# Performance work log

Hardware: AMD Instinct MI355X
Metric: run time of the kernel (lower is better)

The kernel has to match this reference:

```python
import jax, jax.numpy as jnp
import numpy as np

B, S, H, U = 32, 4096, 512, 512


def setup_inputs() -> dict:
    key = jax.random.key(0)
    ks = jax.random.split(key, 6)
    scale = 1.0 / np.sqrt(H)
    return {
        "query": jax.random.normal(ks[0], (B, H), dtype=jnp.float32),
        "values": jax.random.normal(ks[1], (B, S, H), dtype=jnp.float32),
        "W1": jax.random.normal(ks[2], (H, U), dtype=jnp.float32) * scale,
        "b1": jnp.zeros((U,), dtype=jnp.float32),
        "W2": jax.random.normal(ks[3], (H, U), dtype=jnp.float32) * scale,
        "b2": jnp.zeros((U,), dtype=jnp.float32),
        "va": jax.random.normal(ks[4], (U, 1), dtype=jnp.float32) * (1.0 / np.sqrt(U)),
        "bva": jnp.zeros((1,), dtype=jnp.float32),
    }


def reference(query, values, W1, b1, W2, b2, va, bva):
    # query: [B, H] -> [B, 1, U]; values: [B, S, H] -> [B, S, U]
    q_proj = jnp.einsum('bh,hu->bu', query, W1) + b1           # [B, U]
    v_proj = jnp.einsum('bsh,hu->bsu', values, W2) + b2        # [B, S, U]
    scores = jnp.einsum('bsu,uo->bso', jnp.tanh(q_proj[:, None, :] + v_proj), va) + bva  # [B, S, 1]
    attention_weights = jax.nn.softmax(scores, axis=1)         # [B, S, 1]
    context_vector = jnp.sum(attention_weights * values, axis=1)  # [B, H]
    return attention_weights, context_vector
```

## Files before the change

### kernel.cpp

```cpp
#include <hip/hip_runtime.h>
#include <hip/hip_bf16.h>
#include <stdint.h>

#define B_SZ 32
#define S_SZ 4096
#define H_SZ 512
#define U_SZ 512

typedef __attribute__((ext_vector_type(8))) _Float16 half8;
typedef __attribute__((ext_vector_type(4))) float floatx4;

__device__ __forceinline__ void async_copy16(const void* g, void* l) {
    __builtin_amdgcn_global_load_lds(
        (const __attribute__((address_space(1))) void*)g,
        (__attribute__((address_space(3))) void*)l, 16, 0, 0);
}

__global__ __launch_bounds__(256) void prep_kernel(
    const float* __restrict__ W2, const float* __restrict__ b1,
    const float* __restrict__ b2, const float* __restrict__ bva,
    const float* __restrict__ query, const float* __restrict__ W1,
    _Float16* __restrict__ W2s, float* __restrict__ qpb2,
    float* __restrict__ scores, float* __restrict__ ctx)
{
    const int t = threadIdx.x;
    const int bid = blockIdx.x;
    if (bid < 1024) {
        const int i = bid * 256 + t;
        const int k = i >> 9, n = i & 511;
        W2s[(k >> 5) * 16384 + ((k >> 3) & 3) * 4096 + n * 8 + (k & 7)] =
            (_Float16)W2[i];
    } else if (bid < 1536) {
        scores[(bid - 1024) * 256 + t] = *bva;
    } else if (bid < 1600) {
        ctx[(bid - 1536) * 256 + t] = 0.0f;
    } else {
        const int bq = bid - 1600;
        const int b = bq >> 1, uc = bq & 1;
        const int u = uc * 256 + t;
        const float* q  = query + b * H_SZ;
        const float* Wp = W1 + u;
        float a0 = 0.f, a1 = 0.f, a2 = 0.f, a3 = 0.f;
        for (int k = 0; k < 512; k += 4) {
            a0 = fmaf(q[k],     Wp[(size_t)k * U_SZ],       a0);
            a1 = fmaf(q[k + 1], Wp[(size_t)(k + 1) * U_SZ], a1);
            a2 = fmaf(q[k + 2], Wp[(size_t)(k + 2) * U_SZ], a2);
            a3 = fmaf(q[k + 3], Wp[(size_t)(k + 3) * U_SZ], a3);
        }
        qpb2[b * U_SZ + u] = (a0 + a1) + (a2 + a3) + b1[u] + b2[u];
    }
}

__global__ __launch_bounds__(256, 3) void scores_kernel(
    const float* __restrict__ values, const _Float16* __restrict__ W2s,
    const float* __restrict__ qpb2, const float* __restrict__ va,
    float* __restrict__ scores)
{
    __shared__ __align__(16) float    Albs[2][4096];
    __shared__ __align__(16) _Float16 Blbs[2][4096];
    __shared__ float red[256];

    const int t  = threadIdx.x;
    const int w  = t >> 6, l = t & 63;
    const int c  = l & 15, g4 = l >> 4;
    const int mh = w >> 1, nh = w & 1;
    const int n0 = (blockIdx.x & 3) * 128;
    const int m0 = (blockIdx.x >> 2) * 128;
    const int b  = m0 >> 12;

    floatx4 acc[4][4];
#pragma unroll
    for (int mt = 0; mt < 4; ++mt)
#pragma unroll
        for (int nt = 0; nt < 4; ++nt) acc[mt][nt] = (floatx4)(0.0f);

    const float*    Vb0 = values + (size_t)m0 * H_SZ;
    const _Float16* Wb0 = W2s + n0 * 8;

    auto stage = [&](int kb, int buf) {
        const float* Vb = Vb0 + kb * 32;
#pragma unroll
        for (int i = 0; i < 4; ++i) {
            const int j = t + i * 256;
            const int g = j >> 7, ml = j & 127;
            async_copy16(Vb + (size_t)ml * H_SZ + g * 4, &Albs[buf][j * 4]);
        }
        const _Float16* Wb = Wb0 + kb * 16384;
#pragma unroll
        for (int i = 0; i < 2; ++i) {
            const int j = t + i * 256;
            const int kq = j >> 7, nl = j & 127;
            async_copy16(Wb + kq * 4096 + nl * 8, &Blbs[buf][j * 8]);
        }
    };

    stage(0, 0);
    __syncthreads();

    for (int kb = 0; kb < 16; ++kb) {
        const int cur = kb & 1;
        if (kb < 15) stage(kb + 1, cur ^ 1);
        half8 af[4];
#pragma unroll
        for (int mt = 0; mt < 4; ++mt) {
            const int ml = mh * 64 + mt * 16 + c;
            float4 lo = *(const float4*)&Albs[cur][((2 * g4)     * 128 + ml) * 4];
            float4 hi = *(const float4*)&Albs[cur][((2 * g4 + 1) * 128 + ml) * 4];
            half8 a;
            a[0] = (_Float16)lo.x; a[1] = (_Float16)lo.y;
            a[2] = (_Float16)lo.z; a[3] = (_Float16)lo.w;
            a[4] = (_Float16)hi.x; a[5] = (_Float16)hi.y;
            a[6] = (_Float16)hi.z; a[7] = (_Float16)hi.w;
            af[mt] = a;
        }
        half8 bf[4];
#pragma unroll
        for (int nt = 0; nt < 4; ++nt) {
            const int nl = nh * 64 + nt * 16 + c;
            bf[nt] = *(const half8*)&Blbs[cur][(g4 * 128 + nl) * 8];
        }
#pragma unroll
        for (int mt = 0; mt < 4; ++mt)
#pragma unroll
            for (int nt = 0; nt < 4; ++nt)
                acc[mt][nt] = __builtin_amdgcn_mfma_f32_16x16x32_f16(
                    af[mt], bf[nt], acc[mt][nt], 0, 0, 0);
        __syncthreads();
    }

    float qv2[4], vv[4], vv2[4];
#pragma unroll
    for (int nt = 0; nt < 4; ++nt) {
        const int n = n0 + nh * 64 + nt * 16 + c;
        const float q = qpb2[b * U_SZ + n];
        const float v = va[n];
        qv2[nt] = 2.0f * q;
        vv[nt] = v;
        vv2[nt] = 2.0f * v;
    }
#pragma unroll
    for (int mt = 0; mt < 4; ++mt) {
#pragma unroll
        for (int r = 0; r < 4; ++r) {
            float p = 0.0f;
#pragma unroll
            for (int nt = 0; nt < 4; ++nt) {
                const float ex = __expf(fmaf(acc[mt][nt][r], 2.0f, qv2[nt]));
                const float rc = __builtin_amdgcn_rcpf(ex + 1.0f);
                p = fmaf(-vv2[nt], rc, p + vv[nt]);
            }
            p += __shfl_xor(p, 1);
            p += __shfl_xor(p, 2);
            p += __shfl_xor(p, 4);
            p += __shfl_xor(p, 8);
            if (c == 0)
                red[(mh * 64 + mt * 16 + g4 * 4 + r) * 2 + nh] = p;
        }
    }
    __syncthreads();
    if (t < 128)
        atomicAdd(&scores[m0 + t], red[t * 2] + red[t * 2 + 1]);
}

__global__ __launch_bounds__(1024) void sredux_kernel(
    const float* __restrict__ scores, float* __restrict__ ML)
{
    __shared__ float red[16];
    __shared__ float s_max;
    const int b = blockIdx.x;
    const int t = threadIdx.x;
    float4 v = *(const float4*)(scores + b * S_SZ + t * 4);
    float m = fmaxf(fmaxf(v.x, v.y), fmaxf(v.z, v.w));
#pragma unroll
    for (int o = 32; o > 0; o >>= 1) m = fmaxf(m, __shfl_xor(m, o));
    if ((t & 63) == 0) red[t >> 6] = m;
    __syncthreads();
    if (t == 0) {
        float mm = red[0];
        for (int i = 1; i < 16; ++i) mm = fmaxf(mm, red[i]);
        s_max = mm;
    }
    __syncthreads();
    const float mm = s_max;
    float s = __expf(v.x - mm) + __expf(v.y - mm) +
              __expf(v.z - mm) + __expf(v.w - mm);
#pragma unroll
    for (int o = 32; o > 0; o >>= 1) s += __shfl_xor(s, o);
    if ((t & 63) == 0) red[t >> 6] = s;
    __syncthreads();
    if (t == 0) {
        float ss = 0.0f;
        for (int i = 0; i < 16; ++i) ss += red[i];
        ML[b * 2] = mm;
        ML[b * 2 + 1] = ss;
    }
}

__global__ __launch_bounds__(256) void context_kernel(
    const float* __restrict__ values, const float* __restrict__ scores,
    const float* __restrict__ ML, float* __restrict__ out)
{
    __shared__ float wl[128];
    __shared__ __align__(16) float part[4][512];
    const int sc = blockIdx.x, b = blockIdx.y;
    const int t = threadIdx.x;
    const int s0 = sc * 128;
    const float M = ML[b * 2];
    const float rL = 1.0f / ML[b * 2 + 1];
    if (t < 32) {
        float4 sv = *(const float4*)(scores + b * S_SZ + s0 + t * 4);
        float4 wv;
        wv.x = __expf(sv.x - M) * rL; wv.y = __expf(sv.y - M) * rL;
        wv.z = __expf(sv.z - M) * rL; wv.w = __expf(sv.w - M) * rL;
        *(float4*)&wl[t * 4] = wv;
        *(float4*)(out + b * S_SZ + s0 + t * 4) = wv;
    }
    __syncthreads();

    const int g = t >> 6, l = t & 63;
    const float* vp = values + ((size_t)b * S_SZ + s0 + g * 32) * H_SZ + l * 4;
    float4 a00 = {0,0,0,0}, a01 = {0,0,0,0}, a10 = {0,0,0,0}, a11 = {0,0,0,0};
    for (int i = 0; i < 32; i += 2) {
        const float w0 = wl[g * 32 + i];
        const float w1 = wl[g * 32 + i + 1];
        const float* r0 = vp + (size_t)i * H_SZ;
        const float* r1 = r0 + H_SZ;
        float4 v00 = *(const float4*)(r0);
        float4 v01 = *(const float4*)(r0 + 256);
        float4 v10 = *(const float4*)(r1);
        float4 v11 = *(const float4*)(r1 + 256);
        a00.x = fmaf(w0, v00.x, a00.x); a00.y = fmaf(w0, v00.y, a00.y);
        a00.z = fmaf(w0, v00.z, a00.z); a00.w = fmaf(w0, v00.w, a00.w);
        a01.x = fmaf(w0, v01.x, a01.x); a01.y = fmaf(w0, v01.y, a01.y);
        a01.z = fmaf(w0, v01.z, a01.z); a01.w = fmaf(w0, v01.w, a01.w);
        a10.x = fmaf(w1, v10.x, a10.x); a10.y = fmaf(w1, v10.y, a10.y);
        a10.z = fmaf(w1, v10.z, a10.z); a10.w = fmaf(w1, v10.w, a10.w);
        a11.x = fmaf(w1, v11.x, a11.x); a11.y = fmaf(w1, v11.y, a11.y);
        a11.z = fmaf(w1, v11.z, a11.z); a11.w = fmaf(w1, v11.w, a11.w);
    }
    a00.x += a10.x; a00.y += a10.y; a00.z += a10.z; a00.w += a10.w;
    a01.x += a11.x; a01.y += a11.y; a01.z += a11.z; a01.w += a11.w;
    *(float4*)&part[g][l * 4] = a00;
    *(float4*)&part[g][256 + l * 4] = a01;
    __syncthreads();

    float* ctx = out + B_SZ * S_SZ;
#pragma unroll
    for (int rep = 0; rep < 2; ++rep) {
        const int h = rep * 256 + t;
        const float s = (part[0][h] + part[1][h]) + (part[2][h] + part[3][h]);
        atomicAdd(&ctx[b * H_SZ + h], s);
    }
}

extern "C" void kernel_launch(void* const* d_in, const int* in_sizes, int n_in,
                              void* d_out, int out_size, void* d_ws, size_t ws_size,
                              hipStream_t stream) {
    const float* query  = (const float*)d_in[0];
    const float* values = (const float*)d_in[1];
    const float* W1     = (const float*)d_in[2];
    const float* b1     = (const float*)d_in[3];
    const float* W2     = (const float*)d_in[4];
    const float* b2     = (const float*)d_in[5];
    const float* va     = (const float*)d_in[6];
    const float* bva    = (const float*)d_in[7];
    float* out = (float*)d_out;

    char* ws = (char*)d_ws;
    float*    qpb2   = (float*)ws;
    _Float16* W2s    = (_Float16*)(ws + 65536);
    float*    scores = (float*)(ws + 65536 + 524288);
    float*    ML     = (float*)(ws + 65536 + 2 * 524288);

    float* ctx = out + B_SZ * S_SZ;

    prep_kernel<<<1664, 256, 0, stream>>>(W2, b1, b2, bva, query, W1,
                                          W2s, qpb2, scores, ctx);
    scores_kernel<<<4096, 256, 0, stream>>>(values, W2s, qpb2, va, scores);
    sredux_kernel<<<32, 1024, 0, stream>>>(scores, ML);
    context_kernel<<<dim3(32, 32), 256, 0, stream>>>(values, scores, ML, out);
}
```

Before: 595.9 us.

## Pre-convert values to fp16 once and reuse it in the scores and context kernels

Adds a conversion pass in the prep kernel that writes an fp16 copy of values into the workspace. The scores GEMM is templated so it can stream fp16 A tiles straight into MFMA with half the LDS and no per-tile conversion, and its occupancy hint rises from 3 to 4. A new context kernel reads the fp16 copy. This cuts repeated fp32 traffic and conversion work, at the cost of an extra full pass over values and lower precision in the context sum. The fp16 path is used only when the workspace is large enough; otherwise the old fp32 path runs.

```diff
diff --git a/kernel.cpp b/kernel.cpp
--- a/kernel.cpp
+++ b/kernel.cpp
@@ -17,25 +17,39 @@
 }
 
 __global__ __launch_bounds__(256) void prep_kernel(
-    const float* __restrict__ W2, const float* __restrict__ b1,
-    const float* __restrict__ b2, const float* __restrict__ bva,
-    const float* __restrict__ query, const float* __restrict__ W1,
-    _Float16* __restrict__ W2s, float* __restrict__ qpb2,
-    float* __restrict__ scores, float* __restrict__ ctx)
+    const float* __restrict__ values, const float* __restrict__ W2,
+    const float* __restrict__ b1, const float* __restrict__ b2,
+    const float* __restrict__ bva, const float* __restrict__ query,
+    const float* __restrict__ W1, _Float16* __restrict__ W2s,
+    float* __restrict__ qpb2, float* __restrict__ scores,
+    float* __restrict__ ctx, _Float16* __restrict__ vf16, int nconv)
 {
     const int t = threadIdx.x;
     const int bid = blockIdx.x;
-    if (bid < 1024) {
-        const int i = bid * 256 + t;
+    if (bid < nconv) {
+        const size_t i = ((size_t)bid * 256 + t) * 8;
+        float4 v0 = *(const float4*)(values + i);
+        float4 v1 = *(const float4*)(values + i + 4);
+        half8 h;
+        h[0] = (_Float16)v0.x; h[1] = (_Float16)v0.y;
+        h[2] = (_Float16)v0.z; h[3] = (_Float16)v0.w;
+        h[4] = (_Float16)v1.x; h[5] = (_Float16)v1.y;
+        h[6] = (_Float16)v1.z; h[7] = (_Float16)v1.w;
+        *(half8*)(vf16 + i) = h;
+        return;
+    }
+    const int rb = bid - nconv;
+    if (rb < 1024) {
+        const int i = rb * 256 + t;
         const int k = i >> 9, n = i & 511;
         W2s[(k >> 5) * 16384 + ((k >> 3) & 3) * 4096 + n * 8 + (k & 7)] =
             (_Float16)W2[i];
-    } else if (bid < 1536) {
-        scores[(bid - 1024) * 256 + t] = *bva;
-    } else if (bid < 1600) {
-        ctx[(bid - 1536) * 256 + t] = 0.0f;
+    } else if (rb < 1536) {
+        scores[(rb - 1024) * 256 + t] = *bva;
+    } else if (rb < 1600) {
+        ctx[(rb - 1536) * 256 + t] = 0.0f;
     } else {
-        const int bq = bid - 1600;
+        const int bq = rb - 1600;
         const int b = bq >> 1, uc = bq & 1;
         const int u = uc * 256 + t;
         const float* q  = query + b * H_SZ;
@@ -51,12 +65,13 @@
     }
 }
 
-__global__ __launch_bounds__(256, 3) void scores_kernel(
-    const float* __restrict__ values, const _Float16* __restrict__ W2s,
+template <typename AT>
+__global__ __launch_bounds__(256, 4) void scores_kernel(
+    const AT* __restrict__ A, const _Float16* __restrict__ W2s,
     const float* __restrict__ qpb2, const float* __restrict__ va,
     float* __restrict__ scores)
 {
-    __shared__ __align__(16) float    Albs[2][4096];
+    __shared__ __align__(16) AT       Albs[2][4096];
     __shared__ __align__(16) _Float16 Blbs[2][4096];
     __shared__ float red[256];
 
@@ -74,16 +89,25 @@
 #pragma unroll
         for (int nt = 0; nt < 4; ++nt) acc[mt][nt] = (floatx4)(0.0f);
 
-    const float*    Vb0 = values + (size_t)m0 * H_SZ;
+    const AT*       Ab0 = A + (size_t)m0 * H_SZ;
     const _Float16* Wb0 = W2s + n0 * 8;
 
     auto stage = [&](int kb, int buf) {
-        const float* Vb = Vb0 + kb * 32;
-#pragma unroll
-        for (int i = 0; i < 4; ++i) {
-            const int j = t + i * 256;
-            const int g = j >> 7, ml = j & 127;
-            async_copy16(Vb + (size_t)ml * H_SZ + g * 4, &Albs[buf][j * 4]);
+        const AT* Vb = Ab0 + kb * 32;
+        if constexpr (sizeof(AT) == 4) {
+#pragma unroll
+            for (int i = 0; i < 4; ++i) {
+                const int j = t + i * 256;
+                const int g = j >> 7, ml = j & 127;
+                async_copy16(Vb + (size_t)ml * H_SZ + g * 4, &Albs[buf][j * 4]);
+            }
+        } else {
+#pragma unroll
+            for (int i = 0; i < 2; ++i) {
+                const int j = t + i * 256;
+                const int g = j >> 7, ml = j & 127;
+                async_copy16(Vb + (size_t)ml * H_SZ + g * 8, &Albs[buf][j * 8]);
+            }
         }
         const _Float16* Wb = Wb0 + kb * 16384;
 #pragma unroll
@@ -104,14 +128,18 @@
 #pragma unroll
         for (int mt = 0; mt < 4; ++mt) {
             const int ml = mh * 64 + mt * 16 + c;
-            float4 lo = *(const float4*)&Albs[cur][((2 * g4)     * 128 + ml) * 4];
-            float4 hi = *(const float4*)&Albs[cur][((2 * g4 + 1) * 128 + ml) * 4];
-            half8 a;
-            a[0] = (_Float16)lo.x; a[1] = (_Float16)lo.y;
-            a[2] = (_Float16)lo.z; a[3] = (_Float16)lo.w;
-            a[4] = (_Float16)hi.x; a[5] = (_Float16)hi.y;
-            a[6] = (_Float16)hi.z; a[7] = (_Float16)hi.w;
-            af[mt] = a;
+            if constexpr (sizeof(AT) == 4) {
+                float4 lo = *(const float4*)&Albs[cur][((2 * g4)     * 128 + ml) * 4];
+                float4 hi = *(const float4*)&Albs[cur][((2 * g4 + 1) * 128 + ml) * 4];
+                half8 a;
+                a[0] = (_Float16)lo.x; a[1] = (_Float16)lo.y;
+                a[2] = (_Float16)lo.z; a[3] = (_Float16)lo.w;
+                a[4] = (_Float16)hi.x; a[5] = (_Float16)hi.y;
+                a[6] = (_Float16)hi.z; a[7] = (_Float16)hi.w;
+                af[mt] = a;
+            } else {
+                af[mt] = *(const half8*)&Albs[cur][(g4 * 128 + ml) * 8];
+            }
         }
         half8 bf[4];
 #pragma unroll
@@ -196,7 +224,59 @@
     }
 }
 
-__global__ __launch_bounds__(256) void context_kernel(
+__global__ __launch_bounds__(256) void context_f16_kernel(
+    const _Float16* __restrict__ vf16, const float* __restrict__ scores,
+    const float* __restrict__ ML, float* __restrict__ out)
+{
+    __shared__ float wl[128];
+    __shared__ float part[4][512];
+    const int sc = blockIdx.x, b = blockIdx.y;
+    const int t = threadIdx.x;
+    const int s0 = sc * 128;
+    const float M = ML[b * 2];
+    const float rL = 1.0f / ML[b * 2 + 1];
+    if (t < 32) {
+        float4 sv = *(const float4*)(scores + b * S_SZ + s0 + t * 4);
+        float4 wv;
+        wv.x = __expf(sv.x - M) * rL; wv.y = __expf(sv.y - M) * rL;
+        wv.z = __expf(sv.z - M) * rL; wv.w = __expf(sv.w - M) * rL;
+        *(float4*)&wl[t * 4] = wv;
+        *(float4*)(out + b * S_SZ + s0 + t * 4) = wv;
+    }
+    __syncthreads();
+
+    const int g = t >> 6, l = t & 63;
+    const _Float16* vp = vf16 + ((size_t)b * S_SZ + s0 + g * 32) * H_SZ + l * 8;
+    float a[4][8];
+#pragma unroll
+    for (int u = 0; u < 4; ++u)
+#pragma unroll
+        for (int e = 0; e < 8; ++e) a[u][e] = 0.0f;
+    for (int i = 0; i < 32; i += 4) {
+#pragma unroll
+        for (int u = 0; u < 4; ++u) {
+            const float wu = wl[g * 32 + i + u];
+            half8 hv = *(const half8*)(vp + (size_t)(i + u) * H_SZ);
+#pragma unroll
+            for (int e = 0; e < 8; ++e)
+                a[u][e] = fmaf(wu, (float)hv[e], a[u][e]);
+        }
+    }
+#pragma unroll
+    for (int e = 0; e < 8; ++e)
+        part[g][l * 8 + e] = (a[0][e] + a[1][e]) + (a[2][e] + a[3][e]);
+    __syncthreads();
+
+    float* ctx = out + B_SZ * S_SZ;
+#pragma unroll
+    for (int rep = 0; rep < 2; ++rep) {
+        const int h = rep * 256 + t;
+        const float s = (part[0][h] + part[1][h]) + (part[2][h] + part[3][h]);
+        atomicAdd(&ctx[b * H_SZ + h], s);
+    }
+}
+
+__global__ __launch_bounds__(256) void context_f32_kernel(
     const float* __restrict__ values, const float* __restrict__ scores,
     const float* __restrict__ ML, float* __restrict__ out)
 {
@@ -269,14 +349,27 @@
     char* ws = (char*)d_ws;
     float*    qpb2   = (float*)ws;
     _Float16* W2s    = (_Float16*)(ws + 65536);
-    float*    scores = (float*)(ws + 65536 + 524288);
-    float*    ML     = (float*)(ws + 65536 + 2 * 524288);
+    float*    scores = (float*)(ws + 589824);
+    float*    ML     = (float*)(ws + 1114112);
+    _Float16* vf16   = (_Float16*)(ws + 1118208);
+
+    const size_t NEED = 1118208ull + 134217728ull;
+    const bool f16path = ws_size >= NEED;
+    const int nconv = f16path ? 32768 : 0;
 
     float* ctx = out + B_SZ * S_SZ;
 
-    prep_kernel<<<1664, 256, 0, stream>>>(W2, b1, b2, bva, query, W1,
-                                          W2s, qpb2, scores, ctx);
-    scores_kernel<<<4096, 256, 0, stream>>>(values, W2s, qpb2, va, scores);
+    prep_kernel<<<nconv + 1664, 256, 0, stream>>>(
+        values, W2, b1, b2, bva, query, W1, W2s, qpb2, scores, ctx, vf16, nconv);
+    if (f16path) {
+        scores_kernel<_Float16><<<4096, 256, 0, stream>>>(vf16, W2s, qpb2, va, scores);
+    } else {
+        scores_kernel<float><<<4096, 256, 0, stream>>>(values, W2s, qpb2, va, scores);
+    }
     sredux_kernel<<<32, 1024, 0, stream>>>(scores, ML);
-    context_kernel<<<dim3(32, 32), 256, 0, stream>>>(values, scores, ML, out);
-}
+    if (f16path) {
+        context_f16_kernel<<<dim3(32, 32), 256, 0, stream>>>(vf16, scores, ML, out);
+    } else {
+        context_f32_kernel<<<dim3(32, 32), 256, 0, stream>>>(values, scores, ML, out);
+    }
+}
```

After: 545.9 us. -8.4%, faster.
